# Kernel tuning notes

Measured on AMD Instinct MI355X. Metric: run time of the kernel, lower is better.

Reference implementation:

```python
import jax, jax.numpy as jnp
import numpy as np

N, E, H = 2000, 4096, 256

def setup_inputs() -> dict:
    key = jax.random.key(0)
    ks = jax.random.split(key, 24)
    def rn(k, shape, scale=0.05):
        return jax.random.normal(k, shape, dtype=jnp.float32) * scale
    inp = {
        'x': jax.random.randint(ks[0], (N, 1), 0, 5),
        'pos': rn(ks[1], (N, 3), 1.0),
        'edge_index': jax.random.randint(ks[2], (2, E), 0, N),
        'edge_atr': rn(ks[3], (E, 5), 1.0),
        'emb_table': rn(ks[4], (5, 5), 1.0),
        'lin0_W': rn(ks[5], (H, 8)), 'lin0_b': jnp.zeros((H,), jnp.float32),
        'mlp1_W': rn(ks[6], (128, 5)), 'mlp1_b': jnp.zeros((128,), jnp.float32),
        'mlp2_W': rn(ks[7], (H * H, 128), 0.01), 'mlp2_b': jnp.zeros((H * H,), jnp.float32),
        'conv_b': jnp.zeros((H,), jnp.float32),
        'gru_Wih': rn(ks[8], (3 * H, H)), 'gru_Whh': rn(ks[9], (3 * H, H)),
        'gru_bih': jnp.zeros((3 * H,), jnp.float32), 'gru_bhh': jnp.zeros((3 * H,), jnp.float32),
        'lin1_W': rn(ks[10], (H, 2 * H)), 'lin1_b': jnp.zeros((H,), jnp.float32),
        'lin2_W': rn(ks[11], (242, H)), 'lin2_b': jnp.zeros((242,), jnp.float32),
        'l6_W1': rn(ks[12], (128, 2 * H)), 'l6_b1': jnp.zeros((128,), jnp.float32),
        'bn_g': jnp.ones((128,), jnp.float32), 'bn_b': jnp.zeros((128,), jnp.float32),
        'l6_W2': rn(ks[13], (1, 128)), 'l6_b2': jnp.zeros((1,), jnp.float32),
    }
    return inp

def _gru_step(m, h, Wih, Whh, bih, bhh):
    gi = m @ Wih.T + bih  # [N,3H]
    gh = h @ Whh.T + bhh
    gir, giz, gin = jnp.split(gi, 3, axis=1)
    ghr, ghz, ghn = jnp.split(gh, 3, axis=1)
    r = jax.nn.sigmoid(gir + ghr)
    z = jax.nn.sigmoid(giz + ghz)
    n = jnp.tanh(gin + r * ghn)
    return (1.0 - z) * n + z * h

def reference(x, pos, edge_index, edge_atr, emb_table, lin0_W, lin0_b,
              mlp1_W, mlp1_b, mlp2_W, mlp2_b, conv_b,
              gru_Wih, gru_Whh, gru_bih, gru_bhh,
              lin1_W, lin1_b, lin2_W, lin2_b,
              l6_W1, l6_b1, bn_g, bn_b, l6_W2, l6_b2):
    node_emb = emb_table[x[:, 0]]                      # [N,5]
    in_p = jnp.concatenate([node_emb, pos], axis=1)    # [N,8]
    out = jax.nn.relu(in_p @ lin0_W.T + lin0_b)        # [N,H]
    h = out
    row, col = edge_index[0], edge_index[1]
    # edge-conditioned weights (edge_atr is loop-invariant -> compute once)
    he = jax.nn.relu(edge_atr @ mlp1_W.T + mlp1_b)     # [E,128]
    W_e = (he @ mlp2_W.T + mlp2_b).reshape(E, H, H)    # [E,H,H]
    counts = jnp.clip(jax.ops.segment_sum(jnp.ones((E,), jnp.float32), col, num_segments=N), 1.0)
    for _ in range(3):
        msg = jnp.einsum('eh,eho->eo', out[row], W_e)  # gather + per-edge matmul
        agg = jax.ops.segment_sum(msg, col, num_segments=N) / counts[:, None] + conv_b
        m = jax.nn.relu(agg)
        h = _gru_step(m, h, gru_Wih, gru_Whh, gru_bih, gru_bhh)
        out = h
    out_concat = jnp.concatenate([out[row], out[col]], axis=1)  # [E,2H]
    o1 = jax.nn.relu(out_concat @ lin1_W.T + lin1_b)
    out2 = o1 @ lin2_W.T + lin2_b                       # [E,242]
    # lin6: Linear -> BatchNorm1d (batch stats, training mode) -> ReLU -> Linear
    h1 = out_concat @ l6_W1.T + l6_b1                   # [E,128]
    mu = jnp.mean(h1, axis=0)
    var = jnp.var(h1, axis=0)
    h1n = (h1 - mu) * jax.lax.rsqrt(var + 1e-5) * bn_g + bn_b
    precs = jax.nn.relu(h1n) @ l6_W2.T + l6_b2          # [E,1]
    return (out2, precs)
```

## Files before the change

### kernel.cpp

```cpp
#include <hip/hip_runtime.h>
#include <hip/hip_bf16.h>

constexpr int N_ = 2000;
constexpr int E_ = 4096;
constexpr int H_ = 256;
constexpr int KH_ = 128;
constexpr int NV_ = H_ * KH_;
constexpr int MPAD_ = 2048;
constexpr int NG_ = 768;
constexpr float VSCALE = 64.f;
constexpr float VSCALE_INV = 1.f / 64.f;

typedef short bf16x8 __attribute__((ext_vector_type(8)));
typedef float f32x4  __attribute__((ext_vector_type(4)));
typedef float f32x2  __attribute__((ext_vector_type(2)));

__device__ __forceinline__ float bf_lo(unsigned u) { return __uint_as_float(u << 16); }
__device__ __forceinline__ float bf_hi(unsigned u) { return __uint_as_float(u & 0xffff0000u); }
__device__ __forceinline__ short bfbits(float f) {
    __hip_bfloat16 b = __float2bfloat16(f);
    return *(short*)&b;
}

#define PIPE_WAIT_ENTER(N_OUTST)                                   \
    asm volatile("s_waitcnt vmcnt(" #N_OUTST ")" ::: "memory");    \
    __builtin_amdgcn_s_barrier();                                  \
    asm volatile("" ::: "memory");                                 \
    __builtin_amdgcn_sched_barrier(0);

#define PIPE_EXIT()                                                \
    __builtin_amdgcn_sched_barrier(0);                             \
    asm volatile("" ::: "memory");                                 \
    __builtin_amdgcn_s_barrier();

__global__ void k_lin0(const int* __restrict__ x, const float* __restrict__ pos,
                       const float* __restrict__ emb, const float* __restrict__ W,
                       const float* __restrict__ b, float* __restrict__ out,
                       __hip_bfloat16* __restrict__ Abf) {
    int n = blockIdx.x, t = threadIdx.x;
    if (n >= N_) { Abf[(size_t)n * H_ + t] = __float2bfloat16(0.f); return; }
    __shared__ float in_p[8];
    if (t < 5) in_p[t] = emb[x[n] * 5 + t];
    else if (t < 8) in_p[t] = pos[n * 3 + (t - 5)];
    __syncthreads();
    float acc = b[t];
#pragma unroll
    for (int i = 0; i < 8; i++) acc += in_p[i] * W[t * 8 + i];
    float v = fmaxf(acc, 0.f);
    out[n * H_ + t] = v;
    Abf[(size_t)n * H_ + t] = __float2bfloat16(v);
}

__global__ void k_he(const float* __restrict__ ea, const float* __restrict__ W,
                     const float* __restrict__ b, float* __restrict__ he) {
    int e = blockIdx.x, t = threadIdx.x;
    __shared__ float a[5];
    if (t < 5) a[t] = ea[e * 5 + t];
    __syncthreads();
    float acc = b[t];
#pragma unroll
    for (int i = 0; i < 5; i++) acc += a[i] * W[t * 5 + i];
    he[e * KH_ + t] = fmaxf(acc, 0.f);
}

__global__ void k_counts(const int* __restrict__ ei, float* __restrict__ counts) {
    int e = blockIdx.x * blockDim.x + threadIdx.x;
    if (e < E_) atomicAdd(&counts[ei[E_ + e]], 1.0f);
}

__global__ void k_trans_bt(const float* __restrict__ W, __hip_bfloat16* __restrict__ Bt) {
    __shared__ float tile[32][68];
    int t = threadIdx.x;
    int n0 = blockIdx.x * 64, k0 = blockIdx.y * 32;
#pragma unroll
    for (int i = 0; i < 2; i++) {
        int idx = t + i * 256;
        int kk = idx >> 4, nn = (idx & 15) * 4;
        float4 f = *(const float4*)&W[(size_t)(k0 + kk) * NV_ + n0 + nn];
        *(float4*)&tile[kk][nn] = f;
    }
    __syncthreads();
#pragma unroll
    for (int i = 0; i < 2; i++) {
        int idx = t + i * 256;
        int nn = idx >> 3, k4 = (idx & 7) * 4;
        short4 s;
        s.x = bfbits(tile[k4 + 0][nn]);
        s.y = bfbits(tile[k4 + 1][nn]);
        s.z = bfbits(tile[k4 + 2][nn]);
        s.w = bfbits(tile[k4 + 3][nn]);
        *(short4*)&Bt[(size_t)(n0 + nn) * H_ + k0 + k4] = s;
    }
}

__global__ void k_prep_w(const float* __restrict__ Wih, const float* __restrict__ Whh,
                         const float* __restrict__ lin1W, const float* __restrict__ l6W1,
                         const float* __restrict__ lin2W, const float* __restrict__ b2,
                         __hip_bfloat16* __restrict__ WihB, __hip_bfloat16* __restrict__ WhhB,
                         __hip_bfloat16* __restrict__ Bpk,
                         __hip_bfloat16* __restrict__ lin2Wb, __hip_bfloat16* __restrict__ BtB) {
    int i = blockIdx.x * 256 + threadIdx.x;
    if (i < NG_ * H_) {
        WihB[i] = __float2bfloat16(Wih[i]);
        WhhB[i] = __float2bfloat16(Whh[i]);
    }
    Bpk[i] = __float2bfloat16(i < 256 * 512 ? lin1W[i] : l6W1[i - 256 * 512]);
    if (i < 128 * 2 * H_) {
        int r = i >> 8, k = i & 255;
        lin2Wb[i] = __float2bfloat16(r < 242 ? lin2W[r * H_ + k] : 0.f);
        int o = i >> 8, h = i & 255;
        BtB[o * H_ + h] = __float2bfloat16(b2[h * H_ + o]);
    }
}

__global__ void k_concat(const int* __restrict__ ei, const float* __restrict__ h,
                         __hip_bfloat16* __restrict__ Cbf) {
    int e = blockIdx.x, t = threadIdx.x;
    int r = ei[e], c = ei[E_ + e];
    Cbf[(size_t)e * 512 + t]       = __float2bfloat16(h[(size_t)r * H_ + t]);
    Cbf[(size_t)e * 512 + 256 + t] = __float2bfloat16(h[(size_t)c * H_ + t]);
}

template <int KD, bool RELU, bool OUT_BF16>
__global__ __launch_bounds__(256, 3) void k_gemm_nt(const __hip_bfloat16* __restrict__ A,
                                                    const __hip_bfloat16* __restrict__ Bt,
                                                    float* __restrict__ Cf,
                                                    __hip_bfloat16* __restrict__ Cb,
                                                    const float* __restrict__ bias,
                                                    int ldc, int ncols, int mvalid) {
    __shared__ __align__(16) short As[2][4096];
    __shared__ __align__(16) short Bs[2][4096];
    int t = threadIdx.x;
    int lane = t & 63, wave = t >> 6;
    int wm = wave >> 1, wn = wave & 1;
    int quad = lane >> 4, l16 = lane & 15;
    int row0 = blockIdx.y * 128, col0 = blockIdx.x * 128;

    f32x4 acc[4][4] = {};
    int r_ld = (lane >> 2);
    int koff = (((lane & 3) ^ ((lane >> 3) & 3)) * 8);
    int swz = (l16 >> 1) & 3;
    constexpr int NST = KD / 32;

    auto stage = [&](int buf, int k0) {
#pragma unroll
        for (int c = 0; c < 4; c++) {
            int q = wave * 4 + c;
            int ch = q & 7;
            int r = ch * 16 + r_ld;
            const __hip_bfloat16* gp;
            short* lp;
            if (q < 8) { gp = A  + (size_t)(row0 + r) * KD + k0 + koff; lp = &As[buf][ch * 512]; }
            else       { gp = Bt + (size_t)(col0 + r) * KD + k0 + koff; lp = &Bs[buf][ch * 512]; }
            __builtin_amdgcn_global_load_lds(
                (const __attribute__((address_space(1))) unsigned int*)(uintptr_t)gp,
                (__attribute__((address_space(3))) unsigned int*)(uintptr_t)lp,
                16, 0, 0);
        }
    };

    stage(0, 0);
    for (int kk = 0; kk < NST; kk++) {
        int cur = kk & 1;
        if (kk + 1 < NST) {
            stage(cur ^ 1, (kk + 1) * 32);
            PIPE_WAIT_ENTER(4)
        } else {
            PIPE_WAIT_ENTER(0)
        }
        bf16x8 a[4], b[4];
#pragma unroll
        for (int i = 0; i < 4; i++)
            a[i] = *(const bf16x8*)&As[cur][(wm * 64 + i * 16 + l16) * 32 + ((quad ^ swz) << 3)];
#pragma unroll
        for (int j = 0; j < 4; j++)
            b[j] = *(const bf16x8*)&Bs[cur][(wn * 64 + j * 16 + l16) * 32 + ((quad ^ swz) << 3)];
#pragma unroll
        for (int i = 0; i < 4; i++)
#pragma unroll
            for (int j = 0; j < 4; j++)
                acc[i][j] = __builtin_amdgcn_mfma_f32_16x16x32_bf16(a[i], b[j], acc[i][j], 0, 0, 0);
        PIPE_EXIT()
    }

#pragma unroll
    for (int i = 0; i < 4; i++) {
        int gm0 = row0 + wm * 64 + i * 16 + quad * 4;
#pragma unroll
        for (int r = 0; r < 4; r++) {
            int gm = gm0 + r;
            if (gm < mvalid) {
#pragma unroll
                for (int j = 0; j < 4; j++) {
                    int col = col0 + wn * 64 + l16 + j * 16;
                    if (col < ncols) {
                        float v = acc[i][j][r];
                        if (bias) v += bias[col];
                        if (RELU) v = fmaxf(v, 0.f);
                        if (OUT_BF16) Cb[(size_t)gm * ldc + col] = __float2bfloat16(v);
                        else          Cf[(size_t)gm * ldc + col] = v;
                    }
                }
            }
        }
    }
}

__global__ __launch_bounds__(256, 4) void k_gemm_VP(const __hip_bfloat16* __restrict__ Abf,
                                                    const __hip_bfloat16* __restrict__ Bt,
                                                    const __hip_bfloat16* __restrict__ WhhB,
                                                    const __hip_bfloat16* __restrict__ BtB,
                                                    const float* __restrict__ bhh,
                                                    float* __restrict__ gh,
                                                    float* __restrict__ outb,
                                                    unsigned char* __restrict__ V8) {
    __shared__ __align__(16) short As[2][4096];
    __shared__ __align__(16) short Bs[2][4096];
    int bid = blockIdx.x;
    int t = threadIdx.x;
    int lane = t & 63, wave = t >> 6;
    int wm = wave >> 1, wn = wave & 1;
    int quad = lane >> 4, l16 = lane & 15;
    int r_ld = (lane >> 2);
    int koff = (((lane & 3) ^ ((lane >> 3) & 3)) * 8);
    int swz = (l16 >> 1) & 3;

    if (bid < 128) {
        int pbx = bid & 7, pby = bid >> 3;
        bool ob = (pbx >= 6);
        const __hip_bfloat16* Bp = ob ? BtB : WhhB;
        int col0 = ob ? (pbx - 6) * 128 : pbx * 128;
        int ldc = ob ? H_ : NG_;
        float* C = ob ? outb : gh;
        int row0 = pby * 128;

        f32x4 acc[4][4] = {};
        auto stage = [&](int buf, int k0) {
#pragma unroll
            for (int c = 0; c < 4; c++) {
                int q = wave * 4 + c;
                int ch = q & 7;
                int r = ch * 16 + r_ld;
                const __hip_bfloat16* gp;
                short* lp;
                if (q < 8) { gp = Abf + ((size_t)(row0 + r) << 8) + k0 + koff; lp = &As[buf][ch * 512]; }
                else       { gp = Bp  + ((size_t)(col0 + r) << 8) + k0 + koff; lp = &Bs[buf][ch * 512]; }
                __builtin_amdgcn_global_load_lds(
                    (const __attribute__((address_space(1))) unsigned int*)(uintptr_t)gp,
                    (__attribute__((address_space(3))) unsigned int*)(uintptr_t)lp,
                    16, 0, 0);
            }
        };
        stage(0, 0);
        for (int kk = 0; kk < 8; kk++) {
            int cur = kk & 1;
            if (kk + 1 < 8) {
                stage(cur ^ 1, (kk + 1) * 32);
                PIPE_WAIT_ENTER(4)
            } else {
                PIPE_WAIT_ENTER(0)
            }
            bf16x8 a[4], b[4];
#pragma unroll
            for (int i = 0; i < 4; i++)
                a[i] = *(const bf16x8*)&As[cur][(wm * 64 + i * 16 + l16) * 32 + ((quad ^ swz) << 3)];
#pragma unroll
            for (int j = 0; j < 4; j++)
                b[j] = *(const bf16x8*)&Bs[cur][(wn * 64 + j * 16 + l16) * 32 + ((quad ^ swz) << 3)];
#pragma unroll
            for (int i = 0; i < 4; i++)
#pragma unroll
                for (int j = 0; j < 4; j++)
                    acc[i][j] = __builtin_amdgcn_mfma_f32_16x16x32_bf16(a[i], b[j], acc[i][j], 0, 0, 0);
            PIPE_EXIT()
        }
#pragma unroll
        for (int i = 0; i < 4; i++) {
            int gm0 = row0 + wm * 64 + i * 16 + quad * 4;
#pragma unroll
            for (int r = 0; r < 4; r++) {
                int gm = gm0 + r;
                if (gm < N_) {
#pragma unroll
                    for (int j = 0; j < 4; j++) {
                        int col = col0 + wn * 64 + l16 + j * 16;
                        float v = acc[i][j][r] + (ob ? 0.f : bhh[col]);
                        C[(size_t)gm * ldc + col] = v;
                    }
                }
            }
        }
        return;
    }

    int vb = bid - 128;
    int bx = vb & 255, by = vb >> 8;
    int row0 = by * 128, col0 = bx * 128;
    int obase = bx * 8;
    int kb = (bx >> 5) * 16;
    short* Ps = &As[0][0];

    f32x4 acc[4][4] = {};
    auto stage = [&](int buf, int k0) {
#pragma unroll
        for (int c = 0; c < 4; c++) {
            int q = wave * 4 + c;
            int ch = q & 7;
            const __hip_bfloat16* gp;
            short* lp;
            if (q < 8) {
                gp = Abf + ((size_t)(row0 + ch * 16 + r_ld) << 8) + k0 + koff;
                lp = &As[buf][ch * 512];
            } else {
                int nv = ((obase + ch) & 255) * 128 + kb + r_ld;
                gp = Bt + ((size_t)nv << 8) + k0 + koff;
                lp = &Bs[buf][ch * 512];
            }
            __builtin_amdgcn_global_load_lds(
                (const __attribute__((address_space(1))) unsigned int*)(uintptr_t)gp,
                (__attribute__((address_space(3))) unsigned int*)(uintptr_t)lp,
                16, 0, 0);
        }
    };
    stage(0, 0);
    for (int kk = 0; kk < 8; kk++) {
        int cur = kk & 1;
        if (kk + 1 < 8) {
            stage(cur ^ 1, (kk + 1) * 32);
            PIPE_WAIT_ENTER(4)
        } else {
            PIPE_WAIT_ENTER(0)
        }
        bf16x8 a[4], b[4];
#pragma unroll
        for (int i = 0; i < 4; i++)
            a[i] = *(const bf16x8*)&As[cur][(wm * 64 + i * 16 + l16) * 32 + ((quad ^ swz) << 3)];
#pragma unroll
        for (int j = 0; j < 4; j++)
            b[j] = *(const bf16x8*)&Bs[cur][(wn * 64 + j * 16 + l16) * 32 + ((quad ^ swz) << 3)];
#pragma unroll
        for (int i = 0; i < 4; i++)
#pragma unroll
            for (int j = 0; j < 4; j++)
                acc[i][j] = __builtin_amdgcn_mfma_f32_16x16x32_bf16(a[i], b[j], acc[i][j], 0, 0, 0);
        PIPE_EXIT()
    }

#pragma unroll
    for (int pp = 0; pp < 4; pp++) {
        if (wm == (pp >> 1)) {
#pragma unroll
            for (int ii = 0; ii < 2; ii++) {
                const int i = (pp & 1) * 2 + ii;
                int lr = ii * 16 + quad * 4;
#pragma unroll
                for (int r = 0; r < 4; r++) {
#pragma unroll
                    for (int j = 0; j < 4; j++) {
                        int col = wn * 64 + j * 16 + l16;
                        Ps[(lr + r) * 136 + col] = bfbits(acc[i][j][r] * VSCALE);
                    }
                }
            }
        }
        __syncthreads();
        {
            int row = t >> 3;
            int col = (t & 7) * 16;
            int gm = row0 + pp * 32 + row;
            if (gm < N_) {
                uint4 ua = *(const uint4*)&Ps[row * 136 + col];
                uint4 ub = *(const uint4*)&Ps[row * 136 + col + 8];
                unsigned p0 = __builtin_amdgcn_cvt_pk_fp8_f32(bf_lo(ua.x), bf_hi(ua.x), 0, false);
                p0 = __builtin_amdgcn_cvt_pk_fp8_f32(bf_lo(ua.y), bf_hi(ua.y), p0, true);
                unsigned p1 = __builtin_amdgcn_cvt_pk_fp8_f32(bf_lo(ua.z), bf_hi(ua.z), 0, false);
                p1 = __builtin_amdgcn_cvt_pk_fp8_f32(bf_lo(ua.w), bf_hi(ua.w), p1, true);
                unsigned p2 = __builtin_amdgcn_cvt_pk_fp8_f32(bf_lo(ub.x), bf_hi(ub.x), 0, false);
                p2 = __builtin_amdgcn_cvt_pk_fp8_f32(bf_lo(ub.y), bf_hi(ub.y), p2, true);
                unsigned p3 = __builtin_amdgcn_cvt_pk_fp8_f32(bf_lo(ub.z), bf_hi(ub.z), 0, false);
                p3 = __builtin_amdgcn_cvt_pk_fp8_f32(bf_lo(ub.w), bf_hi(ub.w), p3, true);
                uint4 o4;
                o4.x = p0; o4.y = p1; o4.z = p2; o4.w = p3;
                *(uint4*)(V8 + (size_t)gm * NV_ + col0 + col) = o4;
            }
        }
        __syncthreads();
    }
}

__global__ __launch_bounds__(256, 3) void k_gemm_gi(const float* __restrict__ agg,
                                                    const float* __restrict__ counts,
                                                    const float* __restrict__ conv_b,
                                                    const __hip_bfloat16* __restrict__ WihB,
                                                    const float* __restrict__ bih,
                                                    float* __restrict__ gi) {
    __shared__ __align__(16) short As[2][4096];
    __shared__ __align__(16) short Bs[2][4096];
    __shared__ __align__(16) float conv_lds[256];
    int t = threadIdx.x;
    int lane = t & 63, wave = t >> 6;
    int wm = wave >> 1, wn = wave & 1;
    int quad = lane >> 4, l16 = lane & 15;
    int row0 = blockIdx.y * 128, col0 = blockIdx.x * 128;
    int r_ld = (lane >> 2);
    int koff = (((lane & 3) ^ ((lane >> 3) & 3)) * 8);
    int swz = (l16 >> 1) & 3;

    conv_lds[t] = conv_b[t];
    __syncthreads();

    f32x4 acc[4][4] = {};
    float rcv[2];
    const float* asrc[2];
#pragma unroll
    for (int c = 0; c < 2; c++) {
        int ch = wave * 2 + c;
        int row = row0 + ch * 16 + r_ld;
        int rowc = row < N_ ? row : N_ - 1;
        rcv[c] = 1.f / fmaxf(counts[rowc], 1.f);
        asrc[c] = agg + (size_t)rowc * 256;
    }
    float4 R[2][2][2];

    auto loadA = [&](int buf, int k0) {
#pragma unroll
        for (int c = 0; c < 2; c++) {
            R[buf][c][0] = *(const float4*)(asrc[c] + k0 + koff);
            R[buf][c][1] = *(const float4*)(asrc[c] + k0 + koff + 4);
        }
    };
    auto stageB = [&](int buf, int k0) {
#pragma unroll
        for (int c = 0; c < 2; c++) {
            int ch = wave * 2 + c;
            const __hip_bfloat16* gp = WihB + (size_t)(col0 + ch * 16 + r_ld) * 256 + k0 + koff;
            short* lp = &Bs[buf][ch * 512];
            __builtin_amdgcn_global_load_lds(
                (const __attribute__((address_space(1))) unsigned int*)(uintptr_t)gp,
                (__attribute__((address_space(3))) unsigned int*)(uintptr_t)lp,
                16, 0, 0);
        }
    };
    auto writeA = [&](int buf, int k0) {
        float4 cb0 = *(const float4*)&conv_lds[k0 + koff];
        float4 cb1 = *(const float4*)&conv_lds[k0 + koff + 4];
#pragma unroll
        for (int c = 0; c < 2; c++) {
            int ch = wave * 2 + c;
            float rc = rcv[c];
            float4 a0 = R[buf][c][0], a1 = R[buf][c][1];
            bf16x8 v;
            v[0] = bfbits(fmaxf(a0.x * rc + cb0.x, 0.f));
            v[1] = bfbits(fmaxf(a0.y * rc + cb0.y, 0.f));
            v[2] = bfbits(fmaxf(a0.z * rc + cb0.z, 0.f));
            v[3] = bfbits(fmaxf(a0.w * rc + cb0.w, 0.f));
            v[4] = bfbits(fmaxf(a1.x * rc + cb1.x, 0.f));
            v[5] = bfbits(fmaxf(a1.y * rc + cb1.y, 0.f));
            v[6] = bfbits(fmaxf(a1.z * rc + cb1.z, 0.f));
            v[7] = bfbits(fmaxf(a1.w * rc + cb1.w, 0.f));
            *(bf16x8*)&As[buf][ch * 512 + lane * 8] = v;
        }
    };

    loadA(0, 0);
    stageB(0, 0);
#pragma unroll
    for (int kk = 0; kk < 8; kk++) {
        const int cur = kk & 1;
        if (kk + 1 < 8) {
            loadA(cur ^ 1, (kk + 1) * 32);
            stageB(cur ^ 1, (kk + 1) * 32);
        }
        writeA(cur, kk * 32);
        if (kk + 1 < 8) { asm volatile("s_waitcnt vmcnt(6)" ::: "memory"); }
        else            { asm volatile("s_waitcnt vmcnt(0)" ::: "memory"); }
        asm volatile("s_waitcnt lgkmcnt(0)" ::: "memory");
        __builtin_amdgcn_s_barrier();
        asm volatile("" ::: "memory");
        __builtin_amdgcn_sched_barrier(0);
        bf16x8 a[4], b[4];
#pragma unroll
        for (int i = 0; i < 4; i++)
            a[i] = *(const bf16x8*)&As[cur][(wm * 64 + i * 16 + l16) * 32 + ((quad ^ swz) << 3)];
#pragma unroll
        for (int j = 0; j < 4; j++)
            b[j] = *(const bf16x8*)&Bs[cur][(wn * 64 + j * 16 + l16) * 32 + ((quad ^ swz) << 3)];
#pragma unroll
        for (int i = 0; i < 4; i++)
#pragma unroll
            for (int j = 0; j < 4; j++)
                acc[i][j] = __builtin_amdgcn_mfma_f32_16x16x32_bf16(a[i], b[j], acc[i][j], 0, 0, 0);
        PIPE_EXIT()
    }

#pragma unroll
    for (int i = 0; i < 4; i++) {
        int gm0 = row0 + wm * 64 + i * 16 + quad * 4;
#pragma unroll
        for (int r = 0; r < 4; r++) {
            int gm = gm0 + r;
            if (gm < N_) {
#pragma unroll
                for (int j = 0; j < 4; j++) {
                    int col = col0 + wn * 64 + l16 + j * 16;
                    gi[(size_t)gm * NG_ + col] = acc[i][j][r] + bih[col];
                }
            }
        }
    }
}

__global__ __launch_bounds__(256, 3) void k_gemm_tail(const __hip_bfloat16* __restrict__ A,
                                                      const __hip_bfloat16* __restrict__ Bpk,
                                                      const float* __restrict__ b1,
                                                      const float* __restrict__ b2,
                                                      __hip_bfloat16* __restrict__ o1bf,
                                                      float* __restrict__ h1) {
    __shared__ __align__(16) short As[2][4096];
    __shared__ __align__(16) short Bs[2][4096];
    int t = threadIdx.x;
    int lane = t & 63, wave = t >> 6;
    int wm = wave >> 1, wn = wave & 1;
    int quad = lane >> 4, l16 = lane & 15;
    int row0 = blockIdx.y * 128, col0 = blockIdx.x * 128;

    f32x4 acc[4][4] = {};
    int r_ld = (lane >> 2);
    int koff = (((lane & 3) ^ ((lane >> 3) & 3)) * 8);
    int swz = (l16 >> 1) & 3;

    auto stage = [&](int buf, int k0) {
#pragma unroll
        for (int c = 0; c < 4; c++) {
            int q = wave * 4 + c;
            int ch = q & 7;
            int r = ch * 16 + r_ld;
            const __hip_bfloat16* gp;
            short* lp;
            if (q < 8) { gp = A   + (size_t)(row0 + r) * 512 + k0 + koff; lp = &As[buf][ch * 512]; }
            else       { gp = Bpk + (size_t)(col0 + r) * 512 + k0 + koff; lp = &Bs[buf][ch * 512]; }
            __builtin_amdgcn_global_load_lds(
                (const __attribute__((address_space(1))) unsigned int*)(uintptr_t)gp,
                (__attribute__((address_space(3))) unsigned int*)(uintptr_t)lp,
                16, 0, 0);
        }
    };

    stage(0, 0);
    for (int kk = 0; kk < 16; kk++) {
        int cur = kk & 1;
        if (kk + 1 < 16) {
            stage(cur ^ 1, (kk + 1) * 32);
            PIPE_WAIT_ENTER(4)
        } else {
            PIPE_WAIT_ENTER(0)
        }
        bf16x8 a[4], b[4];
#pragma unroll
        for (int i = 0; i < 4; i++)
            a[i] = *(const bf16x8*)&As[cur][(wm * 64 + i * 16 + l16) * 32 + ((quad ^ swz) << 3)];
#pragma unroll
        for (int j = 0; j < 4; j++)
            b[j] = *(const bf16x8*)&Bs[cur][(wn * 64 + j * 16 + l16) * 32 + ((quad ^ swz) << 3)];
#pragma unroll
        for (int i = 0; i < 4; i++)
#pragma unroll
            for (int j = 0; j < 4; j++)
                acc[i][j] = __builtin_amdgcn_mfma_f32_16x16x32_bf16(a[i], b[j], acc[i][j], 0, 0, 0);
        PIPE_EXIT()
    }

#pragma unroll
    for (int i = 0; i < 4; i++) {
        int gm0 = row0 + wm * 64 + i * 16 + quad * 4;
#pragma unroll
        for (int r = 0; r < 4; r++) {
            int gm = gm0 + r;
#pragma unroll
            for (int j = 0; j < 4; j++) {
                int col = col0 + wn * 64 + l16 + j * 16;
                float v = acc[i][j][r];
                if (col < 256) {
                    v = fmaxf(v + b1[col], 0.f);
                    o1bf[(size_t)gm * H_ + col] = __float2bfloat16(v);
                } else {
                    h1[(size_t)gm * 128 + (col - 256)] = v + b2[col - 256];
                }
            }
        }
    }
}

__global__ void k_msg(const int* __restrict__ ei, const float* __restrict__ he,
                      const unsigned char* __restrict__ V8, const float* __restrict__ outb,
                      float* __restrict__ agg) {
    int e = blockIdx.x, o = threadIdx.x;
    __shared__ float hs[KH_];
    if (o < KH_) hs[o] = he[e * KH_ + o] * VSCALE_INV;
    __syncthreads();
    int r = ei[e], c = ei[E_ + e];
    float acc = outb[(size_t)r * H_ + o];
    const unsigned char* vbase = V8 + (size_t)r * NV_ + o * 16;
#pragma unroll
    for (int q = 0; q < 8; q++) {
        uint4 u = *(const uint4*)(vbase + (size_t)q * 4096);
        const float* hp = hs + q * 16;
        f32x2 f;
        f = __builtin_amdgcn_cvt_pk_f32_fp8(u.x, false); acc += hp[0]  * f.x + hp[1]  * f.y;
        f = __builtin_amdgcn_cvt_pk_f32_fp8(u.x, true);  acc += hp[2]  * f.x + hp[3]  * f.y;
        f = __builtin_amdgcn_cvt_pk_f32_fp8(u.y, false); acc += hp[4]  * f.x + hp[5]  * f.y;
        f = __builtin_amdgcn_cvt_pk_f32_fp8(u.y, true);  acc += hp[6]  * f.x + hp[7]  * f.y;
        f = __builtin_amdgcn_cvt_pk_f32_fp8(u.z, false); acc += hp[8]  * f.x + hp[9]  * f.y;
        f = __builtin_amdgcn_cvt_pk_f32_fp8(u.z, true);  acc += hp[10] * f.x + hp[11] * f.y;
        f = __builtin_amdgcn_cvt_pk_f32_fp8(u.w, false); acc += hp[12] * f.x + hp[13] * f.y;
        f = __builtin_amdgcn_cvt_pk_f32_fp8(u.w, true);  acc += hp[14] * f.x + hp[15] * f.y;
    }
    atomicAdd(&agg[(size_t)c * H_ + o], acc);
}

__global__ void k_gru_update(const float* __restrict__ gi, const float* __restrict__ gh,
                             float* __restrict__ h, __hip_bfloat16* __restrict__ Abf,
                             float* __restrict__ agg) {
    int i = blockIdx.x * blockDim.x + threadIdx.x;
    if (i >= N_ * H_) return;
    int n = i >> 8, j = i & 255;
    const float* gip = gi + (size_t)n * NG_;
    const float* ghp = gh + (size_t)n * NG_;
    float r = 1.f / (1.f + expf(-(gip[j] + ghp[j])));
    float z = 1.f / (1.f + expf(-(gip[H_ + j] + ghp[H_ + j])));
    float nn = tanhf(gip[2 * H_ + j] + r * ghp[2 * H_ + j]);
    float hv = (1.f - z) * nn + z * h[i];
    h[i] = hv;
    Abf[i] = __float2bfloat16(hv);
    agg[i] = 0.f;
}

__global__ void k_bnstats(const float* __restrict__ h1, float* __restrict__ mu,
                          float* __restrict__ rsig) {
    int j = blockIdx.x, t = threadIdx.x;
    float s = 0.f, ss = 0.f;
    for (int e = t; e < E_; e += 256) {
        float v = h1[(size_t)e * 128 + j];
        s += v;
        ss += v * v;
    }
    __shared__ float rs[256], rss[256];
    rs[t] = s; rss[t] = ss;
    __syncthreads();
    for (int off = 128; off > 0; off >>= 1) {
        if (t < off) { rs[t] += rs[t + off]; rss[t] += rss[t + off]; }
        __syncthreads();
    }
    if (t == 0) {
        float m_ = rs[0] / E_;
        float v_ = rss[0] / E_ - m_ * m_;
        mu[j] = m_;
        rsig[j] = rsqrtf(v_ + 1e-5f);
    }
}

__global__ void k_precs(const float* __restrict__ h1, const float* __restrict__ mu,
                        const float* __restrict__ rsig, const float* __restrict__ g,
                        const float* __restrict__ bb, const float* __restrict__ W2,
                        const float* __restrict__ b2, float* __restrict__ out) {
    int e = blockIdx.x * blockDim.x + threadIdx.x;
    if (e >= E_) return;
    float acc = b2[0];
#pragma unroll 4
    for (int j = 0; j < 128; j++) {
        float v = (h1[(size_t)e * 128 + j] - mu[j]) * rsig[j] * g[j] + bb[j];
        acc += fmaxf(v, 0.f) * W2[j];
    }
    out[(size_t)E_ * 242 + e] = acc;
}

extern "C" void kernel_launch(void* const* d_in, const int* in_sizes, int n_in,
                              void* d_out, int out_size, void* d_ws, size_t ws_size,
                              hipStream_t stream) {
    const int*   x        = (const int*)  d_in[0];
    const float* pos      = (const float*)d_in[1];
    const int*   ei       = (const int*)  d_in[2];
    const float* edge_atr = (const float*)d_in[3];
    const float* emb      = (const float*)d_in[4];
    const float* lin0_W   = (const float*)d_in[5];
    const float* lin0_b   = (const float*)d_in[6];
    const float* mlp1_W   = (const float*)d_in[7];
    const float* mlp1_b   = (const float*)d_in[8];
    const float* mlp2_W   = (const float*)d_in[9];
    const float* mlp2_b   = (const float*)d_in[10];
    const float* conv_b   = (const float*)d_in[11];
    const float* gru_Wih  = (const float*)d_in[12];
    const float* gru_Whh  = (const float*)d_in[13];
    const float* gru_bih  = (const float*)d_in[14];
    const float* gru_bhh  = (const float*)d_in[15];
    const float* lin1_W   = (const float*)d_in[16];
    const float* lin1_b   = (const float*)d_in[17];
    const float* lin2_W   = (const float*)d_in[18];
    const float* lin2_b   = (const float*)d_in[19];
    const float* l6_W1    = (const float*)d_in[20];
    const float* l6_b1    = (const float*)d_in[21];
    const float* bn_g     = (const float*)d_in[22];
    const float* bn_b     = (const float*)d_in[23];
    const float* l6_W2    = (const float*)d_in[24];
    const float* l6_b2    = (const float*)d_in[25];
    float* out = (float*)d_out;

    char* w = (char*)d_ws;
    size_t off = 0;
    auto alloc = [&](size_t bytes) -> void* {
        void* p = w + off;
        off = (off + bytes + 255) & ~(size_t)255;
        return p;
    };
    float* hbuf   = (float*)alloc((size_t)N_ * H_ * 4);
    float* aggm   = (float*)alloc((size_t)N_ * H_ * 4);
    float* outb   = (float*)alloc((size_t)N_ * H_ * 4);
    float* he     = (float*)alloc((size_t)E_ * KH_ * 4);
    float* gi     = (float*)alloc((size_t)N_ * NG_ * 4);
    float* gh     = (float*)alloc((size_t)N_ * NG_ * 4);
    float* h1     = (float*)alloc((size_t)E_ * 128 * 4);
    float* counts = (float*)alloc((size_t)N_ * 4);
    float* mu     = (float*)alloc(128 * 4);
    float* rsig   = (float*)alloc(128 * 4);
    unsigned char* V8      = (unsigned char*)alloc((size_t)N_ * NV_);
    __hip_bfloat16* Abf    = (__hip_bfloat16*)alloc((size_t)MPAD_ * H_ * 2);
    __hip_bfloat16* Bt     = (__hip_bfloat16*)alloc((size_t)NV_ * H_ * 2);
    __hip_bfloat16* WihB   = (__hip_bfloat16*)alloc((size_t)NG_ * H_ * 2);
    __hip_bfloat16* WhhB   = (__hip_bfloat16*)alloc((size_t)NG_ * H_ * 2);
    __hip_bfloat16* Bpk    = (__hip_bfloat16*)alloc((size_t)384 * 512 * 2);
    __hip_bfloat16* lin2Wb = (__hip_bfloat16*)alloc((size_t)H_ * H_ * 2);
    __hip_bfloat16* BtB    = (__hip_bfloat16*)alloc((size_t)H_ * H_ * 2);
    __hip_bfloat16* Cbf    = (__hip_bfloat16*)alloc((size_t)E_ * 2 * H_ * 2);
    __hip_bfloat16* o1bf   = (__hip_bfloat16*)alloc((size_t)E_ * H_ * 2);

    k_lin0<<<MPAD_, 256, 0, stream>>>(x, pos, emb, lin0_W, lin0_b, hbuf, Abf);
    k_he<<<E_, 128, 0, stream>>>(edge_atr, mlp1_W, mlp1_b, he);
    hipMemsetAsync(counts, 0, (size_t)N_ * 4, stream);
    hipMemsetAsync(aggm, 0, (size_t)N_ * H_ * 4, stream);
    k_counts<<<(E_ + 255) / 256, 256, 0, stream>>>(ei, counts);
    k_trans_bt<<<dim3(NV_ / 64, H_ / 32), 256, 0, stream>>>(mlp2_W, Bt);
    k_prep_w<<<768, 256, 0, stream>>>(gru_Wih, gru_Whh, lin1_W, l6_W1, lin2_W, mlp2_b,
                                      WihB, WhhB, Bpk, lin2Wb, BtB);

    for (int it = 0; it < 3; it++) {
        k_gemm_VP<<<128 + (NV_ / 128) * (MPAD_ / 128), 256, 0, stream>>>(
            Abf, Bt, WhhB, BtB, gru_bhh, gh, outb, V8);
        k_msg<<<E_, 256, 0, stream>>>(ei, he, V8, outb, aggm);
        k_gemm_gi<<<dim3(6, MPAD_ / 128), 256, 0, stream>>>(
            aggm, counts, conv_b, WihB, gru_bih, gi);
        k_gru_update<<<(N_ * H_ + 255) / 256, 256, 0, stream>>>(gi, gh, hbuf, Abf, aggm);
    }

    k_concat<<<E_, 256, 0, stream>>>(ei, hbuf, Cbf);
    k_gemm_tail<<<dim3(3, E_ / 128), 256, 0, stream>>>(Cbf, Bpk, lin1_b, l6_b1, o1bf, h1);
    k_gemm_nt<256, false, false><<<dim3(2, E_ / 128), 256, 0, stream>>>(
        o1bf, lin2Wb, out, nullptr, lin2_b, 242, 242, E_);
    k_bnstats<<<128, 256, 0, stream>>>(h1, mu, rsig);
    k_precs<<<(E_ + 255) / 256, 256, 0, stream>>>(h1, mu, rsig, bn_g, bn_b, l6_W2, l6_b2, out);
}
```

Baseline: 446.7 us.

## Sort edges by source for message locality and fuse setup and BN-stats kernels

Builds a CSR-style ordering of edges by source node (degree count, single-block scan, fill) and has k_msg process edges in that order, interleaved across 8 strided groups, so blocks reading the same node's V8 row run close together and reuse cache. Splits the per-edge dot product into four independent accumulators with loads issued up front. Zero-initialisation of counts and aggm and the count atomics move into k_lin0 and k_he, removing two memsets and a kernel. BatchNorm statistics are accumulated with atomics in the tail GEMM epilogue, removing the separate stats kernel, at the cost of atomic-order nondeterminism and added setup kernels.

Result: faster. 422.4 us (-5.4%).

```diff
diff --git a/kernel.cpp b/kernel.cpp
--- a/kernel.cpp
+++ b/kernel.cpp
@@ -36,9 +36,15 @@
 __global__ void k_lin0(const int* __restrict__ x, const float* __restrict__ pos,
                        const float* __restrict__ emb, const float* __restrict__ W,
                        const float* __restrict__ b, float* __restrict__ out,
-                       __hip_bfloat16* __restrict__ Abf) {
+                       __hip_bfloat16* __restrict__ Abf,
+                       float* __restrict__ counts, float* __restrict__ aggm,
+                       int* __restrict__ deg, int* __restrict__ wcur) {
     int n = blockIdx.x, t = threadIdx.x;
     if (n >= N_) { Abf[(size_t)n * H_ + t] = __float2bfloat16(0.f); return; }
+    if (t == 0) counts[n] = 0.f;
+    if (t == 1) deg[n] = 0;
+    if (t == 2) wcur[n] = 0;
+    aggm[(size_t)n * H_ + t] = 0.f;
     __shared__ float in_p[8];
     if (t < 5) in_p[t] = emb[x[n] * 5 + t];
     else if (t < 8) in_p[t] = pos[n * 3 + (t - 5)];
@@ -52,10 +58,14 @@
 }
 
 __global__ void k_he(const float* __restrict__ ea, const float* __restrict__ W,
-                     const float* __restrict__ b, float* __restrict__ he) {
+                     const float* __restrict__ b, float* __restrict__ he,
+                     const int* __restrict__ ei, float* __restrict__ counts,
+                     int* __restrict__ deg) {
     int e = blockIdx.x, t = threadIdx.x;
     __shared__ float a[5];
     if (t < 5) a[t] = ea[e * 5 + t];
+    if (t == 8) atomicAdd(&counts[ei[E_ + e]], 1.0f);
+    if (t == 9) atomicAdd(&deg[ei[e]], 1);
     __syncthreads();
     float acc = b[t];
 #pragma unroll
@@ -63,9 +73,43 @@
     he[e * KH_ + t] = fmaxf(acc, 0.f);
 }
 
-__global__ void k_counts(const int* __restrict__ ei, float* __restrict__ counts) {
+__global__ void k_scan(const int* __restrict__ deg, int* __restrict__ rowptr) {
+    __shared__ int ws[256];
+    int t = threadIdx.x;
+    int base = t * 8;
+    int loc[8];
+    int s = 0;
+#pragma unroll
+    for (int j = 0; j < 8; j++) {
+        int idx = base + j;
+        int d = (idx < N_) ? deg[idx] : 0;
+        loc[j] = s;
+        s += d;
+    }
+    ws[t] = s;
+    __syncthreads();
+    for (int off2 = 1; off2 < 256; off2 <<= 1) {
+        int v = (t >= off2) ? ws[t - off2] : 0;
+        __syncthreads();
+        ws[t] += v;
+        __syncthreads();
+    }
+    int excl = ws[t] - s;
+#pragma unroll
+    for (int j = 0; j < 8; j++) {
+        int idx = base + j;
+        if (idx <= N_) rowptr[idx] = excl + loc[j];
+    }
+}
+
+__global__ void k_fill(const int* __restrict__ ei, const int* __restrict__ rowptr,
+                       int* __restrict__ wcur, int* __restrict__ eord) {
     int e = blockIdx.x * blockDim.x + threadIdx.x;
-    if (e < E_) atomicAdd(&counts[ei[E_ + e]], 1.0f);
+    if (e < E_) {
+        int r = ei[e];
+        int p = atomicAdd(&wcur[r], 1);
+        eord[rowptr[r] + p] = e;
+    }
 }
 
 __global__ void k_trans_bt(const float* __restrict__ W, __hip_bfloat16* __restrict__ Bt) {
@@ -114,8 +158,9 @@
 }
 
 __global__ void k_concat(const int* __restrict__ ei, const float* __restrict__ h,
-                         __hip_bfloat16* __restrict__ Cbf) {
+                         __hip_bfloat16* __restrict__ Cbf, float* __restrict__ bnsum) {
     int e = blockIdx.x, t = threadIdx.x;
+    if (e == 0) bnsum[t] = 0.f;
     int r = ei[e], c = ei[E_ + e];
     Cbf[(size_t)e * 512 + t]       = __float2bfloat16(h[(size_t)r * H_ + t]);
     Cbf[(size_t)e * 512 + 256 + t] = __float2bfloat16(h[(size_t)c * H_ + t]);
@@ -515,7 +560,8 @@
                                                       const float* __restrict__ b1,
                                                       const float* __restrict__ b2,
                                                       __hip_bfloat16* __restrict__ o1bf,
-                                                      float* __restrict__ h1) {
+                                                      float* __restrict__ h1,
+                                                      float* __restrict__ bnsum) {
     __shared__ __align__(16) short As[2][4096];
     __shared__ __align__(16) short Bs[2][4096];
     int t = threadIdx.x;
@@ -589,32 +635,80 @@
             }
         }
     }
-}
-
-__global__ void k_msg(const int* __restrict__ ei, const float* __restrict__ he,
+
+    if (col0 == 256) {
+#pragma unroll
+        for (int j = 0; j < 4; j++) {
+            int cj = wn * 64 + j * 16 + l16;
+            float bj = b2[cj];
+            float s = 0.f, ss = 0.f;
+#pragma unroll
+            for (int i = 0; i < 4; i++)
+#pragma unroll
+                for (int r = 0; r < 4; r++) {
+                    float v = acc[i][j][r] + bj;
+                    s += v;
+                    ss += v * v;
+                }
+            s  += __shfl_xor(s, 16);  s  += __shfl_xor(s, 32);
+            ss += __shfl_xor(ss, 16); ss += __shfl_xor(ss, 32);
+            if (quad == 0) {
+                atomicAdd(&bnsum[cj], s);
+                atomicAdd(&bnsum[128 + cj], ss);
+            }
+        }
+    }
+}
+
+__global__ void k_msg(const int* __restrict__ ei, const int* __restrict__ eord,
+                      const float* __restrict__ he,
                       const unsigned char* __restrict__ V8, const float* __restrict__ outb,
                       float* __restrict__ agg) {
-    int e = blockIdx.x, o = threadIdx.x;
+    int bid = blockIdx.x;
+    int e = eord[((bid & 7) << 9) | (bid >> 3)];
+    int o = threadIdx.x;
     __shared__ float hs[KH_];
     if (o < KH_) hs[o] = he[e * KH_ + o] * VSCALE_INV;
     __syncthreads();
     int r = ei[e], c = ei[E_ + e];
-    float acc = outb[(size_t)r * H_ + o];
     const unsigned char* vbase = V8 + (size_t)r * NV_ + o * 16;
-#pragma unroll
-    for (int q = 0; q < 8; q++) {
-        uint4 u = *(const uint4*)(vbase + (size_t)q * 4096);
-        const float* hp = hs + q * 16;
+
+    auto dot16 = [&](uint4 u, const float* hp) -> float {
         f32x2 f;
-        f = __builtin_amdgcn_cvt_pk_f32_fp8(u.x, false); acc += hp[0]  * f.x + hp[1]  * f.y;
-        f = __builtin_amdgcn_cvt_pk_f32_fp8(u.x, true);  acc += hp[2]  * f.x + hp[3]  * f.y;
-        f = __builtin_amdgcn_cvt_pk_f32_fp8(u.y, false); acc += hp[4]  * f.x + hp[5]  * f.y;
-        f = __builtin_amdgcn_cvt_pk_f32_fp8(u.y, true);  acc += hp[6]  * f.x + hp[7]  * f.y;
-        f = __builtin_amdgcn_cvt_pk_f32_fp8(u.z, false); acc += hp[8]  * f.x + hp[9]  * f.y;
-        f = __builtin_amdgcn_cvt_pk_f32_fp8(u.z, true);  acc += hp[10] * f.x + hp[11] * f.y;
-        f = __builtin_amdgcn_cvt_pk_f32_fp8(u.w, false); acc += hp[12] * f.x + hp[13] * f.y;
-        f = __builtin_amdgcn_cvt_pk_f32_fp8(u.w, true);  acc += hp[14] * f.x + hp[15] * f.y;
-    }
+        float s;
+        f = __builtin_amdgcn_cvt_pk_f32_fp8(u.x, false); s  = hp[0]  * f.x + hp[1]  * f.y;
+        f = __builtin_amdgcn_cvt_pk_f32_fp8(u.x, true);  s += hp[2]  * f.x + hp[3]  * f.y;
+        f = __builtin_amdgcn_cvt_pk_f32_fp8(u.y, false); s += hp[4]  * f.x + hp[5]  * f.y;
+        f = __builtin_amdgcn_cvt_pk_f32_fp8(u.y, true);  s += hp[6]  * f.x + hp[7]  * f.y;
+        f = __builtin_amdgcn_cvt_pk_f32_fp8(u.z, false); s += hp[8]  * f.x + hp[9]  * f.y;
+        f = __builtin_amdgcn_cvt_pk_f32_fp8(u.z, true);  s += hp[10] * f.x + hp[11] * f.y;
+        f = __builtin_amdgcn_cvt_pk_f32_fp8(u.w, false); s += hp[12] * f.x + hp[13] * f.y;
+        f = __builtin_amdgcn_cvt_pk_f32_fp8(u.w, true);  s += hp[14] * f.x + hp[15] * f.y;
+        return s;
+    };
+
+    float p0, p1, p2, p3;
+    {
+        uint4 u0 = *(const uint4*)(vbase);
+        uint4 u1 = *(const uint4*)(vbase + 4096);
+        uint4 u2 = *(const uint4*)(vbase + 2 * 4096);
+        uint4 u3 = *(const uint4*)(vbase + 3 * 4096);
+        p0 = dot16(u0, hs);
+        p1 = dot16(u1, hs + 16);
+        p2 = dot16(u2, hs + 32);
+        p3 = dot16(u3, hs + 48);
+    }
+    {
+        uint4 u0 = *(const uint4*)(vbase + 4 * 4096);
+        uint4 u1 = *(const uint4*)(vbase + 5 * 4096);
+        uint4 u2 = *(const uint4*)(vbase + 6 * 4096);
+        uint4 u3 = *(const uint4*)(vbase + 7 * 4096);
+        p0 += dot16(u0, hs + 64);
+        p1 += dot16(u1, hs + 80);
+        p2 += dot16(u2, hs + 96);
+        p3 += dot16(u3, hs + 112);
+    }
+    float acc = outb[(size_t)r * H_ + o] + ((p0 + p1) + (p2 + p3));
     atomicAdd(&agg[(size_t)c * H_ + o], acc);
 }
 
@@ -635,40 +729,25 @@
     agg[i] = 0.f;
 }
 
-__global__ void k_bnstats(const float* __restrict__ h1, float* __restrict__ mu,
-                          float* __restrict__ rsig) {
-    int j = blockIdx.x, t = threadIdx.x;
-    float s = 0.f, ss = 0.f;
-    for (int e = t; e < E_; e += 256) {
-        float v = h1[(size_t)e * 128 + j];
-        s += v;
-        ss += v * v;
-    }
-    __shared__ float rs[256], rss[256];
-    rs[t] = s; rss[t] = ss;
+__global__ void k_precs(const float* __restrict__ h1, const float* __restrict__ bnsum,
+                        const float* __restrict__ g, const float* __restrict__ bb,
+                        const float* __restrict__ W2, const float* __restrict__ b2,
+                        float* __restrict__ out) {
+    __shared__ float smu[128], srs[128];
+    int t = threadIdx.x;
+    if (t < 128) {
+        float mu = bnsum[t] * (1.f / E_);
+        float var = bnsum[128 + t] * (1.f / E_) - mu * mu;
+        smu[t] = mu;
+        srs[t] = rsqrtf(var + 1e-5f);
+    }
     __syncthreads();
-    for (int off = 128; off > 0; off >>= 1) {
-        if (t < off) { rs[t] += rs[t + off]; rss[t] += rss[t + off]; }
-        __syncthreads();
-    }
-    if (t == 0) {
-        float m_ = rs[0] / E_;
-        float v_ = rss[0] / E_ - m_ * m_;
-        mu[j] = m_;
-        rsig[j] = rsqrtf(v_ + 1e-5f);
-    }
-}
-
-__global__ void k_precs(const float* __restrict__ h1, const float* __restrict__ mu,
-                        const float* __restrict__ rsig, const float* __restrict__ g,
-                        const float* __restrict__ bb, const float* __restrict__ W2,
-                        const float* __restrict__ b2, float* __restrict__ out) {
-    int e = blockIdx.x * blockDim.x + threadIdx.x;
+    int e = blockIdx.x * blockDim.x + t;
     if (e >= E_) return;
     float acc = b2[0];
 #pragma unroll 4
     for (int j = 0; j < 128; j++) {
-        float v = (h1[(size_t)e * 128 + j] - mu[j]) * rsig[j] * g[j] + bb[j];
+        float v = (h1[(size_t)e * 128 + j] - smu[j]) * srs[j] * g[j] + bb[j];
         acc += fmaxf(v, 0.f) * W2[j];
     }
     out[(size_t)E_ * 242 + e] = acc;
@@ -720,8 +799,11 @@
     float* gh     = (float*)alloc((size_t)N_ * NG_ * 4);
     float* h1     = (float*)alloc((size_t)E_ * 128 * 4);
     float* counts = (float*)alloc((size_t)N_ * 4);
-    float* mu     = (float*)alloc(128 * 4);
-    float* rsig   = (float*)alloc(128 * 4);
+    float* bnsum  = (float*)alloc(256 * 4);
+    int*   deg    = (int*)  alloc((size_t)N_ * 4);
+    int*   wcur   = (int*)  alloc((size_t)N_ * 4);
+    int*   rowptr = (int*)  alloc((size_t)(N_ + 1) * 4);
+    int*   eord   = (int*)  alloc((size_t)E_ * 4);
     unsigned char* V8      = (unsigned char*)alloc((size_t)N_ * NV_);
     __hip_bfloat16* Abf    = (__hip_bfloat16*)alloc((size_t)MPAD_ * H_ * 2);
     __hip_bfloat16* Bt     = (__hip_bfloat16*)alloc((size_t)NV_ * H_ * 2);
@@ -733,11 +815,11 @@
     __hip_bfloat16* Cbf    = (__hip_bfloat16*)alloc((size_t)E_ * 2 * H_ * 2);
     __hip_bfloat16* o1bf   = (__hip_bfloat16*)alloc((size_t)E_ * H_ * 2);
 
-    k_lin0<<<MPAD_, 256, 0, stream>>>(x, pos, emb, lin0_W, lin0_b, hbuf, Abf);
-    k_he<<<E_, 128, 0, stream>>>(edge_atr, mlp1_W, mlp1_b, he);
-    hipMemsetAsync(counts, 0, (size_t)N_ * 4, stream);
-    hipMemsetAsync(aggm, 0, (size_t)N_ * H_ * 4, stream);
-    k_counts<<<(E_ + 255) / 256, 256, 0, stream>>>(ei, counts);
+    k_lin0<<<MPAD_, 256, 0, stream>>>(x, pos, emb, lin0_W, lin0_b, hbuf, Abf,
+                                      counts, aggm, deg, wcur);
+    k_he<<<E_, 128, 0, stream>>>(edge_atr, mlp1_W, mlp1_b, he, ei, counts, deg);
+    k_scan<<<1, 256, 0, stream>>>(deg, rowptr);
+    k_fill<<<(E_ + 255) / 256, 256, 0, stream>>>(ei, rowptr, wcur, eord);
     k_trans_bt<<<dim3(NV_ / 64, H_ / 32), 256, 0, stream>>>(mlp2_W, Bt);
     k_prep_w<<<768, 256, 0, stream>>>(gru_Wih, gru_Whh, lin1_W, l6_W1, lin2_W, mlp2_b,
                                       WihB, WhhB, Bpk, lin2Wb, BtB);
@@ -745,16 +827,16 @@
     for (int it = 0; it < 3; it++) {
         k_gemm_VP<<<128 + (NV_ / 128) * (MPAD_ / 128), 256, 0, stream>>>(
             Abf, Bt, WhhB, BtB, gru_bhh, gh, outb, V8);
-        k_msg<<<E_, 256, 0, stream>>>(ei, he, V8, outb, aggm);
+        k_msg<<<E_, 256, 0, stream>>>(ei, eord, he, V8, outb, aggm);
         k_gemm_gi<<<dim3(6, MPAD_ / 128), 256, 0, stream>>>(
             aggm, counts, conv_b, WihB, gru_bih, gi);
         k_gru_update<<<(N_ * H_ + 255) / 256, 256, 0, stream>>>(gi, gh, hbuf, Abf, aggm);
     }
 
-    k_concat<<<E_, 256, 0, stream>>>(ei, hbuf, Cbf);
-    k_gemm_tail<<<dim3(3, E_ / 128), 256, 0, stream>>>(Cbf, Bpk, lin1_b, l6_b1, o1bf, h1);
+    k_concat<<<E_, 256, 0, stream>>>(ei, hbuf, Cbf, bnsum);
+    k_gemm_tail<<<dim3(3, E_ / 128), 256, 0, stream>>>(Cbf, Bpk, lin1_b, l6_b1,
+                                                       o1bf, h1, bnsum);
     k_gemm_nt<256, false, false><<<dim3(2, E_ / 128), 256, 0, stream>>>(
         o1bf, lin2Wb, out, nullptr, lin2_b, 242, 242, E_);
-    k_bnstats<<<128, 256, 0, stream>>>(h1, mu, rsig);
-    k_precs<<<(E_ + 255) / 256, 256, 0, stream>>>(h1, mu, rsig, bn_g, bn_b, l6_W2, l6_b2, out);
-}
+    k_precs<<<(E_ + 255) / 256, 256, 0, stream>>>(h1, bnsum, bn_g, bn_b, l6_W2, l6_b2, out);
+}
```
